# Kernel tuning notes

Hardware: AMD Instinct MI355X
Metric: run time of the kernel (lower is better)

The kernel has to match this reference:

```python
import jax, jax.numpy as jnp
import numpy as np

EPS = float(np.finfo(np.float32).eps)


def fake_quant_w(w):
    # per-output-channel symmetric int8 fake quant; w: (out, in)
    w_d = jax.lax.stop_gradient(w)
    max_abs = jnp.max(jnp.abs(w_d), axis=1, keepdims=True)
    scale = jnp.maximum(max_abs / 127.0, EPS)
    w_q = jnp.clip(jnp.round(w_d / scale), -127, 127)
    return w_q * scale


def woq_linear(x, w, b):
    return x @ fake_quant_w(w).T + b


def setup_inputs() -> dict:
    key = jax.random.key(0)
    ks = jax.random.split(key, 9)
    dim = 1024
    B, S = 2, 2048
    def wmat(k):
        return jax.random.normal(k, (dim, dim), dtype=jnp.float32) * (1.0 / np.sqrt(dim))
    def bvec(k):
        return jax.random.normal(k, (dim,), dtype=jnp.float32) * 0.01
    return {
        "x": jax.random.normal(ks[0], (B, S, dim), dtype=jnp.float32),
        "wq": wmat(ks[1]), "bq": bvec(ks[2]),
        "wk": wmat(ks[3]), "bk": bvec(ks[4]),
        "wv": wmat(ks[5]), "bv": bvec(ks[6]),
        "wp": wmat(ks[7]), "bp": bvec(ks[8]),
    }


def reference(x, wq, bq, wk, bk, wv, bv, wp, bp):
    B, S, C = x.shape
    H = 16
    D = C // H
    scale = D ** -0.5
    # QKV projections with fake-quantized weights -> (B, H, S, D)
    q = woq_linear(x, wq, bq).reshape(B, S, H, D).transpose(0, 2, 1, 3)
    k = woq_linear(x, wk, bk).reshape(B, S, H, D).transpose(0, 2, 1, 3)
    v = woq_linear(x, wv, bv).reshape(B, S, H, D).transpose(0, 2, 1, 3)
    attn = jnp.einsum("bhsd,bhtd->bhst", q, k) * scale  # (B,H,S,S)
    attn = jax.nn.softmax(attn, axis=-1)
    out = jnp.einsum("bhst,bhtd->bhsd", attn, v)
    out = out.transpose(0, 2, 1, 3).reshape(B, S, C)
    return woq_linear(out, wp, bp)
```

## Files before the change

kernel.cpp:

```cpp
#include <hip/hip_runtime.h>
#include <stdint.h>

typedef short bf16x8 __attribute__((ext_vector_type(8)));
typedef float f32x4 __attribute__((ext_vector_type(4)));
typedef uint16_t u16;
typedef uint32_t u32;
typedef u16 u16x4 __attribute__((ext_vector_type(4)));
typedef u32 u32x2 __attribute__((ext_vector_type(2)));
typedef u32 u32x4 __attribute__((ext_vector_type(4)));

#define EPSF 1.1920929e-07f

static __device__ __forceinline__ u16 f2bf(float f) {
  union { float f; uint32_t u; } v; v.f = f;
  return (u16)((v.u + 0x7FFFu + ((v.u >> 16) & 1u)) >> 16);
}
static __device__ __forceinline__ float bf2f(u16 h) {
  union { uint32_t u; float f; } v; v.u = ((uint32_t)h) << 16;
  return v.f;
}
static __device__ __forceinline__ float exp2_fast(float x) {
  return __builtin_amdgcn_exp2f(x);
}
static __device__ __forceinline__ u32 cvt_pk_bf16(float lo, float hi) {
  u32 r;
  asm("v_cvt_pk_bf16_f32 %0, %1, %2" : "=v"(r) : "v"(lo), "v"(hi));
  return r;
}
static __device__ __forceinline__ void gload_lds16(const void* g, void* l) {
  __builtin_amdgcn_global_load_lds(
      (const __attribute__((address_space(1))) void*)g,
      (__attribute__((address_space(3))) void*)l, 16, 0, 0);
}
template <int N>
static __device__ __forceinline__ void vmwait() {
  asm volatile("s_waitcnt vmcnt(%0)" ::"i"(N) : "memory");
}

__global__ __launch_bounds__(256) void prep_kernel(
    const float* __restrict__ wq, const float* __restrict__ wk,
    const float* __restrict__ wv, const float* __restrict__ wp,
    const float* __restrict__ x,
    u16* __restrict__ wout, float* __restrict__ scales, u16* __restrict__ xb) {
  const int t = threadIdx.x;
  if (blockIdx.x < 4096) {
    const int row = blockIdx.x & 1023;
    const int mat = blockIdx.x >> 10;
    const float* W = (mat == 0) ? wq : (mat == 1) ? wk : (mat == 2) ? wv : wp;
    const float4 v = ((const float4*)(W + (size_t)row * 1024))[t];
    float m = fmaxf(fmaxf(fabsf(v.x), fabsf(v.y)), fmaxf(fabsf(v.z), fabsf(v.w)));
#pragma unroll
    for (int off = 1; off < 64; off <<= 1) m = fmaxf(m, __shfl_xor(m, off));
    __shared__ float red[4];
    if ((t & 63) == 0) red[t >> 6] = m;
    __syncthreads();
    m = fmaxf(fmaxf(red[0], red[1]), fmaxf(red[2], red[3]));
    const float scale = fmaxf(m / 127.0f, EPSF);
    float q0 = fminf(fmaxf(rintf(v.x / scale), -127.f), 127.f);
    float q1 = fminf(fmaxf(rintf(v.y / scale), -127.f), 127.f);
    float q2 = fminf(fmaxf(rintf(v.z / scale), -127.f), 127.f);
    float q3 = fminf(fmaxf(rintf(v.w / scale), -127.f), 127.f);
    u16x4 o; o.x = f2bf(q0); o.y = f2bf(q1); o.z = f2bf(q2); o.w = f2bf(q3);
    *(u16x4*)(wout + ((size_t)(mat * 1024 + row)) * 1024 + t * 4) = o;
    if (t == 0) scales[mat * 1024 + row] = scale;
  } else {
    const int i = (blockIdx.x - 4096) * 256 + t;
    const float4 v = ((const float4*)x)[i];
    u16x4 hv;
    hv.x = f2bf(v.x); hv.y = f2bf(v.y); hv.z = f2bf(v.z); hv.w = f2bf(v.w);
    *(u16x4*)(xb + (size_t)i * 4) = hv;
  }
}

template <int MODE, int MR, int NR, int NT, int KT, int LDA>
__global__ __launch_bounds__(512) void gemm_kernel(
    const u16* __restrict__ A, const u16* __restrict__ Bw,
    const float* __restrict__ scales, const float* __restrict__ b0,
    const float* __restrict__ b1, const float* __restrict__ b2,
    u16* __restrict__ qkv, float* __restrict__ outp) {
  constexpr int BM = 2 * MR * 16;
  constexpr int BN = 4 * NR * 16;
  constexpr int OPS = BM / 64 + BN / 64;
  __shared__ u16 As[2][BM * 64];
  __shared__ u16 Bs[2][BN * 64];
  const int tid = threadIdx.x;
  const int w = tid >> 6, l = tid & 63;
  const int per = gridDim.x >> 3;
  const int L = (blockIdx.x & 7) * per + (blockIdx.x >> 3);
  const int tile_n = (L % NT) * BN;
  const int tile_m = (L / NT) * BM;
  const int wm = w >> 2, wn = w & 3;
  const int l15 = l & 15, l4 = l >> 4;
  const int sw = l15 & 7;

  f32x4 acc[MR][NR];
  const f32x4 vzero = {0.f, 0.f, 0.f, 0.f};
#pragma unroll
  for (int m = 0; m < MR; ++m)
#pragma unroll
    for (int n = 0; n < NR; ++n) acc[m][n] = vzero;

  const int r8 = tid >> 3;
  const int g = tid & 7;
  const int gs = g ^ (r8 & 7);
  auto STAGE = [&](int slot, int j) {
    const int kb = j * 64;
    const int kbB = kb & 1023;
#pragma unroll
    for (int i = 0; i < BM / 64; ++i)
      gload_lds16(A + (size_t)(tile_m + i * 64 + r8) * LDA + kb + gs * 8,
                  &As[slot][(i * 64 + r8) * 64 + g * 8]);
#pragma unroll
    for (int i = 0; i < BN / 64; ++i)
      gload_lds16(Bw + (size_t)(tile_n + i * 64 + r8) * 1024 + kbB + gs * 8,
                  &Bs[slot][(i * 64 + r8) * 64 + g * 8]);
  };

  STAGE(0, 0);
  STAGE(1, 1);
  vmwait<OPS>();
  __builtin_amdgcn_s_barrier();

  for (int j = 0; j < KT; ++j) {
    const int cur = j & 1;
#pragma unroll
    for (int ks = 0; ks < 2; ++ks) {
      bf16x8 af[MR], bfv[NR];
      const int sg8 = ((ks * 4 + l4) ^ sw) * 8;
#pragma unroll
      for (int m = 0; m < MR; ++m)
        af[m] = *(const bf16x8*)(&As[cur][(wm * (MR * 16) + m * 16 + l15) * 64 + sg8]);
#pragma unroll
      for (int n = 0; n < NR; ++n)
        bfv[n] = *(const bf16x8*)(&Bs[cur][(wn * (NR * 16) + n * 16 + l15) * 64 + sg8]);
      __builtin_amdgcn_s_setprio(1);
#pragma unroll
      for (int m = 0; m < MR; ++m)
#pragma unroll
        for (int n = 0; n < NR; ++n)
          acc[m][n] = __builtin_amdgcn_mfma_f32_16x16x32_bf16(af[m], bfv[n], acc[m][n], 0, 0, 0);
      __builtin_amdgcn_s_setprio(0);
    }
    __builtin_amdgcn_s_barrier();
    if (j + 2 < KT) {
      STAGE(cur, j + 2);
      vmwait<OPS>();
    } else {
      vmwait<0>();
    }
    __builtin_amdgcn_s_barrier();
  }

#pragma unroll
  for (int m = 0; m < MR; ++m) {
#pragma unroll
    for (int n = 0; n < NR; ++n) {
      const int col = tile_n + wn * (NR * 16) + n * 16 + l15;
      const float sc = scales[col];
      if constexpr (MODE == 0) {
        const int mat = col >> 10, oo = col & 1023;
        const float* bias = (mat == 0) ? b0 : (mat == 1) ? b1 : b2;
        const float bb = bias[oo];
        const int hh = oo >> 6, dd = oo & 63;
        if (mat == 2) {
          const int rowm0 = tile_m + wm * (MR * 16) + m * 16 + l4 * 4;
          const int b = rowm0 >> 11, s = rowm0 & 2047;
          u16x4 pk;
#pragma unroll
          for (int jj = 0; jj < 4; ++jj) pk[jj] = f2bf(acc[m][n][jj] * sc + bb);
          *(u16x4*)(qkv + (size_t)2 * 4194304 +
                    ((size_t)(b * 16 + hh) * 64 + dd) * 2048 + s) = pk;
        } else {
#pragma unroll
          for (int jj = 0; jj < 4; ++jj) {
            const int rowm = tile_m + wm * (MR * 16) + m * 16 + l4 * 4 + jj;
            const int b = rowm >> 11, s = rowm & 2047;
            float y = acc[m][n][jj] * sc + bb;
            if (mat == 0) y *= 0.18033688011112042f;
            qkv[(size_t)mat * 4194304 + ((size_t)(b * 16 + hh) * 2048 + s) * 64 + dd] = f2bf(y);
          }
        }
      } else {
        const float bb = b0[col];
#pragma unroll
        for (int jj = 0; jj < 4; ++jj) {
          const int rowm = tile_m + wm * (MR * 16) + m * 16 + l4 * 4 + jj;
          outp[(size_t)rowm * 1024 + col] = acc[m][n][jj] * sc + bb;
        }
      }
    }
  }
}

__global__ __launch_bounds__(512, 4) void attn_kernel(
    const u16* __restrict__ qg, const u16* __restrict__ kg,
    const u16* __restrict__ vtg, u16* __restrict__ po) {
  __shared__ u16 Kt[2][2][64 * 64];
  __shared__ u16 Vt[2][2][64 * 64];
  const int tid = threadIdx.x;
  const int w = tid >> 6, l = tid & 63;
  const int Lb = (blockIdx.x & 7) * 64 + (blockIdx.x >> 3);
  const int bh = Lb >> 4;
  const int qt = Lb & 15;
  const u16* qp = qg + (size_t)bh * 131072;
  const u16* kp = kg + (size_t)bh * 131072;
  const u16* vp = vtg + (size_t)bh * 131072;
  const int wg = w & 3, grp = w >> 2;
  const int qrow0 = qt * 128 + wg * 32;
  const int l15 = l & 15, l4 = l >> 4;
  const int sw = l15 & 7;

  const int sr = tid >> 3, sg = tid & 7;
  const int gsw = (sg ^ (sr & 7)) << 3;
  auto STAGE = [&](const int slot, const int j) {
    const int kA = j * 64, kB = 1024 + j * 64;
    gload_lds16(kp + (size_t)(kA + sr) * 64 + gsw, &Kt[slot][0][tid * 8]);
    gload_lds16(vp + (size_t)sr * 2048 + kA + gsw, &Vt[slot][0][tid * 8]);
    gload_lds16(kp + (size_t)(kB + sr) * 64 + gsw, &Kt[slot][1][tid * 8]);
    gload_lds16(vp + (size_t)sr * 2048 + kB + gsw, &Vt[slot][1][tid * 8]);
  };

  bf16x8 qfr[2][2];
#pragma unroll
  for (int dk = 0; dk < 2; ++dk)
#pragma unroll
    for (int qf = 0; qf < 2; ++qf)
      qfr[dk][qf] =
          *(const bf16x8*)(qp + (size_t)(qrow0 + qf * 16 + l15) * 64 + dk * 32 + l4 * 8);

  const f32x4 vzero = {0.f, 0.f, 0.f, 0.f};
  f32x4 O[4][2];
#pragma unroll
  for (int di = 0; di < 4; ++di)
#pragma unroll
    for (int qf = 0; qf < 2; ++qf) O[di][qf] = vzero;
  float lrun[2] = {0.f, 0.f};

  auto DO_ITER = [&](const int slot, const int j) {
    const u16* Kb = &Kt[slot][grp][0];
    const u16* Vb = &Vt[slot][grp][0];

    f32x4 sfr[2][4];
#pragma unroll
    for (int qf = 0; qf < 2; ++qf)
#pragma unroll
      for (int ki = 0; ki < 4; ++ki) sfr[qf][ki] = vzero;
#pragma unroll
    for (int dk = 0; dk < 2; ++dk) {
      bf16x8 kf[4];
#pragma unroll
      for (int ki = 0; ki < 4; ++ki)
        kf[ki] = *(const bf16x8*)(Kb + (ki * 16 + l15) * 64 + (((dk * 4 + l4) ^ sw) << 3));
      __builtin_amdgcn_s_setprio(1);
#pragma unroll
      for (int ki = 0; ki < 4; ++ki)
#pragma unroll
        for (int qf = 0; qf < 2; ++qf)
          sfr[qf][ki] = __builtin_amdgcn_mfma_f32_16x16x32_bf16(kf[ki], qfr[dk][qf], sfr[qf][ki], 0, 0, 0);
      __builtin_amdgcn_s_setprio(0);
    }

    u32 pw[2][8];
#pragma unroll
    for (int qf = 0; qf < 2; ++qf) {
      float rs = 0.f;
#pragma unroll
      for (int ki = 0; ki < 4; ++ki) {
        const f32x4 s4 = sfr[qf][ki];
        const float p0 = exp2_fast(s4[0]);
        const float p1 = exp2_fast(s4[1]);
        const float p2 = exp2_fast(s4[2]);
        const float p3 = exp2_fast(s4[3]);
        rs += (p0 + p1) + (p2 + p3);
        pw[qf][ki * 2 + 0] = cvt_pk_bf16(p0, p1);
        pw[qf][ki * 2 + 1] = cvt_pk_bf16(p2, p3);
      }
      lrun[qf] += rs;
    }

#pragma unroll
    for (int kkl = 0; kkl < 2; ++kkl) {
      const u32x4 t0 = {pw[0][kkl * 4 + 0], pw[0][kkl * 4 + 1],
                        pw[0][kkl * 4 + 2], pw[0][kkl * 4 + 3]};
      const u32x4 t1 = {pw[1][kkl * 4 + 0], pw[1][kkl * 4 + 1],
                        pw[1][kkl * 4 + 2], pw[1][kkl * 4 + 3]};
      const bf16x8 pf0 = __builtin_bit_cast(bf16x8, t0);
      const bf16x8 pf1 = __builtin_bit_cast(bf16x8, t1);
      const int o0 = (((kkl * 4 + (l4 >> 1)) ^ sw) << 3) + (l4 & 1) * 4;
      const int o1 = (((kkl * 4 + 2 + (l4 >> 1)) ^ sw) << 3) + (l4 & 1) * 4;
      bf16x8 vf[4];
#pragma unroll
      for (int di = 0; di < 4; ++di) {
        const u16* vrow = Vb + (di * 16 + l15) * 64;
        const u32x2 lo = *(const u32x2*)(vrow + o0);
        const u32x2 hi = *(const u32x2*)(vrow + o1);
        const u32x4 q = {lo.x, lo.y, hi.x, hi.y};
        vf[di] = __builtin_bit_cast(bf16x8, q);
      }
      __builtin_amdgcn_s_setprio(1);
#pragma unroll
      for (int di = 0; di < 4; ++di) {
        O[di][0] = __builtin_amdgcn_mfma_f32_16x16x32_bf16(pf0, vf[di], O[di][0], 0, 0, 0);
        O[di][1] = __builtin_amdgcn_mfma_f32_16x16x32_bf16(pf1, vf[di], O[di][1], 0, 0, 0);
      }
      __builtin_amdgcn_s_setprio(0);
    }

    __builtin_amdgcn_s_barrier();
    if (j + 2 < 16) {
      STAGE(slot, j + 2);
      vmwait<4>();
    } else {
      vmwait<0>();
    }
    __builtin_amdgcn_s_barrier();
  };

  STAGE(0, 0);
  STAGE(1, 1);
  vmwait<4>();
  __builtin_amdgcn_s_barrier();

  for (int jp = 0; jp < 8; ++jp) {
    DO_ITER(0, jp * 2);
    DO_ITER(1, jp * 2 + 1);
  }

  float* Osh = (float*)&Kt[0][0][0];
  float* lsh = (float*)&Vt[0][0][0];
  if (grp == 1) {
#pragma unroll
    for (int qf = 0; qf < 2; ++qf) {
      float* ob = Osh + (wg * 2 + qf) * 1024;
#pragma unroll
      for (int di = 0; di < 4; ++di)
#pragma unroll
        for (int jj = 0; jj < 4; ++jj)
          ob[(l4 * 4 + jj) * 64 + di * 16 + l15] = O[di][qf][jj];
      lsh[(wg * 2 + qf) * 64 + l] = lrun[qf];
    }
  }
  __syncthreads();
  if (grp == 0) {
    const int b = bh >> 4, hh = bh & 15;
#pragma unroll
    for (int qf = 0; qf < 2; ++qf) {
      lrun[qf] += lsh[(wg * 2 + qf) * 64 + l];
      lrun[qf] += __shfl_xor(lrun[qf], 16);
      lrun[qf] += __shfl_xor(lrun[qf], 32);
    }
#pragma unroll
    for (int qf = 0; qf < 2; ++qf) {
      float lq[4];
#pragma unroll
      for (int jj = 0; jj < 4; ++jj)
        lq[jj] = __builtin_amdgcn_rcpf(__shfl(lrun[qf], l4 * 4 + jj));
      const float* ob = Osh + (wg * 2 + qf) * 1024;
#pragma unroll
      for (int di = 0; di < 4; ++di)
#pragma unroll
        for (int jj = 0; jj < 4; ++jj) {
          const float oval =
              (O[di][qf][jj] + ob[(l4 * 4 + jj) * 64 + di * 16 + l15]) * lq[jj];
          const int srw = qrow0 + qf * 16 + l4 * 4 + jj;
          const int c = hh * 64 + di * 16 + l15;
          po[((size_t)(b * 2048 + srw)) * 1024 + c] = f2bf(oval);
        }
    }
  }
}

extern "C" void kernel_launch(void* const* d_in, const int* in_sizes, int n_in,
                              void* d_out, int out_size, void* d_ws, size_t ws_size,
                              hipStream_t stream) {
  (void)in_sizes; (void)n_in; (void)out_size; (void)ws_size;
  const float* x  = (const float*)d_in[0];
  const float* wq = (const float*)d_in[1];
  const float* bq = (const float*)d_in[2];
  const float* wk = (const float*)d_in[3];
  const float* bk = (const float*)d_in[4];
  const float* wv = (const float*)d_in[5];
  const float* bv = (const float*)d_in[6];
  const float* wp = (const float*)d_in[7];
  const float* bp = (const float*)d_in[8];

  char* ws = (char*)d_ws;
  u16*   wquant = (u16*)ws;
  float* scales = (float*)(ws + 8388608);
  u16*   xb     = (u16*)(ws + 8404992);
  u16*   po     = xb;
  u16*   qkv    = (u16*)(ws + 25182208);

  prep_kernel<<<dim3(8192), dim3(256), 0, stream>>>(
      wq, wk, wv, wp, x, wquant, scales, xb);
  gemm_kernel<0, 4, 3, 16, 16, 1024><<<dim3(512), dim3(512), 0, stream>>>(
      xb, wquant, scales, bq, bk, bv, qkv, nullptr);
  attn_kernel<<<dim3(512), dim3(512), 0, stream>>>(
      qkv, qkv + 4194304, qkv + 8388608, po);
  gemm_kernel<1, 2, 2, 8, 16, 1024><<<dim3(512), dim3(512), 0, stream>>>(
      po, wquant + 3145728, scales + 3072, bp, nullptr, nullptr, nullptr, (float*)d_out);
}
```

Measured before the change: 98.64 us.

## Prefetch next KV tile at iteration start and split epilogue across both wave groups

The K/V staging now issues the load for tile j+1 into the other slot at the start of each iteration. It waits for it at the end, which removes the pre-stage barrier and the two-tile lookahead. The final combine is also split so each wave group reduces and writes one of the two query fragments, instead of group 0 doing all the output. The intent is to cut barrier count and balance the epilogue. In exchange prefetch depth drops to one tile, so load latency may be less hidden, and there is a potential WAR hazard on the slot being overwritten while the other group still reads it.

```diff
diff --git a/kernel.cpp b/kernel.cpp
--- a/kernel.cpp
+++ b/kernel.cpp
@@ -237,6 +237,7 @@
   float lrun[2] = {0.f, 0.f};
 
   auto DO_ITER = [&](const int slot, const int j) {
+    if (j + 1 < 16) STAGE(slot ^ 1, j + 1);
     const u16* Kb = &Kt[slot][grp][0];
     const u16* Vb = &Vt[slot][grp][0];
 
@@ -306,19 +307,12 @@
       __builtin_amdgcn_s_setprio(0);
     }
 
-    __builtin_amdgcn_s_barrier();
-    if (j + 2 < 16) {
-      STAGE(slot, j + 2);
-      vmwait<4>();
-    } else {
-      vmwait<0>();
-    }
+    vmwait<0>();
     __builtin_amdgcn_s_barrier();
   };
 
   STAGE(0, 0);
-  STAGE(1, 1);
-  vmwait<4>();
+  vmwait<0>();
   __builtin_amdgcn_s_barrier();
 
   for (int jp = 0; jp < 8; ++jp) {
@@ -329,44 +323,62 @@
   float* Osh = (float*)&Kt[0][0][0];
   float* lsh = (float*)&Vt[0][0][0];
   if (grp == 1) {
-#pragma unroll
-    for (int qf = 0; qf < 2; ++qf) {
-      float* ob = Osh + (wg * 2 + qf) * 1024;
-#pragma unroll
-      for (int di = 0; di < 4; ++di)
-#pragma unroll
-        for (int jj = 0; jj < 4; ++jj)
-          ob[(l4 * 4 + jj) * 64 + di * 16 + l15] = O[di][qf][jj];
-      lsh[(wg * 2 + qf) * 64 + l] = lrun[qf];
-    }
+    float* ob = Osh + (0 * 4 + wg) * 1024;
+#pragma unroll
+    for (int di = 0; di < 4; ++di)
+#pragma unroll
+      for (int jj = 0; jj < 4; ++jj)
+        ob[(l4 * 4 + jj) * 64 + di * 16 + l15] = O[di][0][jj];
+    lsh[(0 * 4 + wg) * 64 + l] = lrun[0];
+  } else {
+    float* ob = Osh + (1 * 4 + wg) * 1024;
+#pragma unroll
+    for (int di = 0; di < 4; ++di)
+#pragma unroll
+      for (int jj = 0; jj < 4; ++jj)
+        ob[(l4 * 4 + jj) * 64 + di * 16 + l15] = O[di][1][jj];
+    lsh[(1 * 4 + wg) * 64 + l] = lrun[1];
   }
   __syncthreads();
+  const int b = bh >> 4, hh = bh & 15;
   if (grp == 0) {
-    const int b = bh >> 4, hh = bh & 15;
-#pragma unroll
-    for (int qf = 0; qf < 2; ++qf) {
-      lrun[qf] += lsh[(wg * 2 + qf) * 64 + l];
-      lrun[qf] += __shfl_xor(lrun[qf], 16);
-      lrun[qf] += __shfl_xor(lrun[qf], 32);
-    }
-#pragma unroll
-    for (int qf = 0; qf < 2; ++qf) {
-      float lq[4];
-#pragma unroll
-      for (int jj = 0; jj < 4; ++jj)
-        lq[jj] = __builtin_amdgcn_rcpf(__shfl(lrun[qf], l4 * 4 + jj));
-      const float* ob = Osh + (wg * 2 + qf) * 1024;
-#pragma unroll
-      for (int di = 0; di < 4; ++di)
-#pragma unroll
-        for (int jj = 0; jj < 4; ++jj) {
-          const float oval =
-              (O[di][qf][jj] + ob[(l4 * 4 + jj) * 64 + di * 16 + l15]) * lq[jj];
-          const int srw = qrow0 + qf * 16 + l4 * 4 + jj;
-          const int c = hh * 64 + di * 16 + l15;
-          po[((size_t)(b * 2048 + srw)) * 1024 + c] = f2bf(oval);
-        }
-    }
+    const float* obr = Osh + (0 * 4 + wg) * 1024;
+    float lt = lrun[0] + lsh[(0 * 4 + wg) * 64 + l];
+    lt += __shfl_xor(lt, 16);
+    lt += __shfl_xor(lt, 32);
+    float lq[4];
+#pragma unroll
+    for (int jj = 0; jj < 4; ++jj)
+      lq[jj] = __builtin_amdgcn_rcpf(__shfl(lt, l4 * 4 + jj));
+#pragma unroll
+    for (int di = 0; di < 4; ++di)
+#pragma unroll
+      for (int jj = 0; jj < 4; ++jj) {
+        const float oval =
+            (O[di][0][jj] + obr[(l4 * 4 + jj) * 64 + di * 16 + l15]) * lq[jj];
+        const int srw = qrow0 + l4 * 4 + jj;
+        const int c = hh * 64 + di * 16 + l15;
+        po[((size_t)(b * 2048 + srw)) * 1024 + c] = f2bf(oval);
+      }
+  } else {
+    const float* obr = Osh + (1 * 4 + wg) * 1024;
+    float lt = lrun[1] + lsh[(1 * 4 + wg) * 64 + l];
+    lt += __shfl_xor(lt, 16);
+    lt += __shfl_xor(lt, 32);
+    float lq[4];
+#pragma unroll
+    for (int jj = 0; jj < 4; ++jj)
+      lq[jj] = __builtin_amdgcn_rcpf(__shfl(lt, l4 * 4 + jj));
+#pragma unroll
+    for (int di = 0; di < 4; ++di)
+#pragma unroll
+      for (int jj = 0; jj < 4; ++jj) {
+        const float oval =
+            (O[di][1][jj] + obr[(l4 * 4 + jj) * 64 + di * 16 + l15]) * lq[jj];
+        const int srw = qrow0 + 16 + l4 * 4 + jj;
+        const int c = hh * 64 + di * 16 + l15;
+        po[((size_t)(b * 2048 + srw)) * 1024 + c] = f2bf(oval);
+      }
   }
 }
 
```

Result: slower. 104.2 us (+5.6%).
